# Performance work log

Hardware: AMD Instinct MI355X
Metric: run time of the kernel (lower is better)

Reference implementation:

```python
import jax, jax.numpy as jnp
import numpy as np

N = 1_000_000
C = 128
NUM_GROUPS = 100_000


def setup_inputs() -> dict:
    key = jax.random.key(0)
    k1, k2, k3 = jax.random.split(key, 3)
    ref_bxyz = jax.random.normal(k1, (N, 4), dtype=jnp.float32)
    ref_feat = jax.random.normal(k2, (N, C), dtype=jnp.float32)
    group_ids = jax.random.randint(k3, (N,), 0, NUM_GROUPS, dtype=jnp.int64)
    return {"ref_bxyz": ref_bxyz, "ref_feat": ref_feat, "group_ids": group_ids}


def reference(ref_bxyz, ref_feat, group_ids):
    # scatter-mean over groups, then gather back to each point
    num_groups = NUM_GROUPS  # static (original uses group_ids.max()+1)
    sums = jax.ops.segment_sum(ref_feat, group_ids, num_segments=num_groups)  # [G, C]
    counts = jax.ops.segment_sum(
        jnp.ones((ref_feat.shape[0],), dtype=ref_feat.dtype), group_ids,
        num_segments=num_groups)  # [G]
    group_mean = sums / jnp.maximum(counts, 1.0)[:, None]  # [G, C]
    return group_mean[group_ids]  # [N, C]
```

## Files before the change

### kernel.cpp

```cpp
#include <hip/hip_runtime.h>

#define NPTS 1000000
#define CH 128
#define NG 100000
#define SCAN_CHUNK 1024
#define NB ((NG + SCAN_CHUNK - 1) / SCAN_CHUNK)


__global__ void hist_kernel(const int* __restrict__ gid, int* __restrict__ cnt) {
    int i = blockIdx.x * blockDim.x + threadIdx.x;
    if (i < NPTS) atomicAdd(&cnt[gid[i]], 1);
}

__global__ void scan_blocks_kernel(const int* __restrict__ cnt, int* __restrict__ off,
                                   int* __restrict__ bsum) {
    __shared__ int lds[256];
    int t = threadIdx.x;
    int base = blockIdx.x * SCAN_CHUNK + t * 4;
    int a0 = 0, a1 = 0, a2 = 0, a3 = 0;
    if (base + 0 < NG) a0 = cnt[base + 0];
    if (base + 1 < NG) a1 = cnt[base + 1];
    if (base + 2 < NG) a2 = cnt[base + 2];
    if (base + 3 < NG) a3 = cnt[base + 3];
    lds[t] = a0 + a1 + a2 + a3;
    __syncthreads();
    for (int d = 1; d < 256; d <<= 1) {
        int v = (t >= d) ? lds[t - d] : 0;
        __syncthreads();
        lds[t] += v;
        __syncthreads();
    }
    int excl = (t == 0) ? 0 : lds[t - 1];
    if (t == 255) bsum[blockIdx.x] = lds[255];
    if (base + 0 < NG) off[base + 0] = excl;
    if (base + 1 < NG) off[base + 1] = excl + a0;
    if (base + 2 < NG) off[base + 2] = excl + a0 + a1;
    if (base + 3 < NG) off[base + 3] = excl + a0 + a1 + a2;
}

__global__ void scan_bsum_kernel(int* __restrict__ bsum) {
    __shared__ int lds[128];
    int t = threadIdx.x;
    int v = (t < NB) ? bsum[t] : 0;
    lds[t] = v;
    __syncthreads();
    for (int d = 1; d < 128; d <<= 1) {
        int u = (t >= d) ? lds[t - d] : 0;
        __syncthreads();
        lds[t] += u;
        __syncthreads();
    }
    int excl = (t == 0) ? 0 : lds[t - 1];
    if (t < NB) bsum[t] = excl;
}

__global__ void fill_kernel(const int* __restrict__ gid, const int* __restrict__ off,
                            const int* __restrict__ bsum, int* __restrict__ cursor,
                            int* __restrict__ idx) {
    int i = blockIdx.x * blockDim.x + threadIdx.x;
    if (i < NPTS) {
        int g = gid[i];
        int s = atomicAdd(&cursor[g], 1);
        idx[off[g] + bsum[g >> 10] + s] = i;
    }
}

__global__ void reduce_kernel(const float* __restrict__ feat, const int* __restrict__ idx,
                              const int* __restrict__ off, const int* __restrict__ bsum,
                              const int* __restrict__ cnt, float* __restrict__ means) {
    long long t = (long long)blockIdx.x * blockDim.x + threadIdx.x;
    int g = (int)(t >> 6);
    int lane = (int)(t & 63);
    if (g >= NG) return;
    int o = off[g] + bsum[g >> 10];
    int n = cnt[g];
    float2 a0 = make_float2(0.f, 0.f), a1 = make_float2(0.f, 0.f);
    int j = 0;
    for (; j + 2 <= n; j += 2) {
        int p0 = idx[o + j];
        int p1 = idx[o + j + 1];
        float2 v0 = ((const float2*)(feat + (long long)p0 * CH))[lane];
        float2 v1 = ((const float2*)(feat + (long long)p1 * CH))[lane];
        a0.x += v0.x; a0.y += v0.y;
        a1.x += v1.x; a1.y += v1.y;
    }
    if (j < n) {
        int p = idx[o + j];
        float2 v = ((const float2*)(feat + (long long)p * CH))[lane];
        a0.x += v.x; a0.y += v.y;
    }
    float inv = 1.0f / fmaxf((float)n, 1.0f);
    float2 r = make_float2((a0.x + a1.x) * inv, (a0.y + a1.y) * inv);
    ((float2*)(means + (long long)g * CH))[lane] = r;
}

__global__ void gather_mean_kernel(const float* __restrict__ means,
                                   const int* __restrict__ gid,
                                   float* __restrict__ out) {
    long long t = (long long)blockIdx.x * blockDim.x + threadIdx.x;
    int point = (int)(t >> 5);
    int sub = (int)(t & 31);
    if (point >= NPTS) return;
    int g = gid[point];
    float4 v = ((const float4*)(means + (long long)g * CH))[sub];
    ((float4*)(out + (long long)point * CH))[sub] = v;
}


__global__ void accum_kernel(const float* __restrict__ feat,
                             const int* __restrict__ gid,
                             float* __restrict__ sums,
                             float* __restrict__ counts) {
    long long t = (long long)blockIdx.x * blockDim.x + threadIdx.x;
    int point = (int)(t >> 5);
    int sub = (int)(t & 31);
    if (point >= NPTS) return;
    int g = gid[point];
    const float4 v = ((const float4*)(feat + (long long)point * CH))[sub];
    float* dst = sums + (long long)g * CH + sub * 4;
    atomicAdd(dst + 0, v.x);
    atomicAdd(dst + 1, v.y);
    atomicAdd(dst + 2, v.z);
    atomicAdd(dst + 3, v.w);
    if (sub == 0) atomicAdd(counts + g, 1.0f);
}

__global__ void inv_kernel(float* __restrict__ counts) {
    int g = blockIdx.x * blockDim.x + threadIdx.x;
    if (g < NG) counts[g] = 1.0f / fmaxf(counts[g], 1.0f);
}

__global__ void gather_kernel(const float* __restrict__ sums,
                              const float* __restrict__ inv,
                              const int* __restrict__ gid,
                              float* __restrict__ out) {
    long long t = (long long)blockIdx.x * blockDim.x + threadIdx.x;
    int point = (int)(t >> 5);
    int sub = (int)(t & 31);
    if (point >= NPTS) return;
    int g = gid[point];
    float ic = inv[g];
    float4 v = ((const float4*)(sums + (long long)g * CH))[sub];
    v.x *= ic; v.y *= ic; v.z *= ic; v.w *= ic;
    ((float4*)(out + (long long)point * CH))[sub] = v;
}


extern "C" void kernel_launch(void* const* d_in, const int* in_sizes, int n_in,
                              void* d_out, int out_size, void* d_ws, size_t ws_size,
                              hipStream_t stream) {
    const float* feat = (const float*)d_in[1];
    const int* gid = (const int*)d_in[2];
    float* out = (float*)d_out;

    char* p = (char*)d_ws;
    float* means = (float*)p;          p += (size_t)NG * CH * sizeof(float);
    int* idx     = (int*)p;            p += (size_t)NPTS * sizeof(int);
    int* cnt     = (int*)p;            p += (size_t)NG * sizeof(int);
    int* off     = (int*)p;            p += (size_t)NG * sizeof(int);
    int* cursor  = (int*)p;            p += (size_t)NG * sizeof(int);
    int* bsum    = (int*)p;            p += 128 * sizeof(int);
    size_t need = (size_t)(p - (char*)d_ws);

    const int block = 256;

    if (ws_size >= need) {
        hipMemsetAsync(cnt, 0, (size_t)NG * sizeof(int) * 3 + 128 * sizeof(int), stream);

        hist_kernel<<<(NPTS + block - 1) / block, block, 0, stream>>>(gid, cnt);
        scan_blocks_kernel<<<NB, 256, 0, stream>>>(cnt, off, bsum);
        scan_bsum_kernel<<<1, 128, 0, stream>>>(bsum);
        fill_kernel<<<(NPTS + block - 1) / block, block, 0, stream>>>(gid, off, bsum, cursor, idx);

        int rgrid = (int)(((long long)NG * 64 + block - 1) / block);
        reduce_kernel<<<rgrid, block, 0, stream>>>(feat, idx, off, bsum, cnt, means);

        int ggrid = (int)(((long long)NPTS * 32 + block - 1) / block);
        gather_mean_kernel<<<ggrid, block, 0, stream>>>(means, gid, out);
    } else {
        float* sums = (float*)d_ws;
        float* counts = sums + (long long)NG * CH;
        size_t zero_bytes = ((size_t)NG * CH + NG) * sizeof(float);
        hipMemsetAsync(d_ws, 0, zero_bytes, stream);

        long long total = (long long)NPTS * 32;
        int grid = (int)((total + block - 1) / block);
        accum_kernel<<<grid, block, 0, stream>>>(feat, gid, sums, counts);
        inv_kernel<<<(NG + block - 1) / block, block, 0, stream>>>(counts);
        gather_kernel<<<grid, block, 0, stream>>>(sums, counts, gid, out);
    }
}
```

Baseline: 1.030 ms.

## Fuse group mean reduction with scatter to output rows, drop means buffer

The reduce kernel now writes each group's mean directly to every member point's output row, eliminating the intermediate means array and the separate gather kernel. Point indices for a group are loaded once per wave and broadcast via shuffles, and group offsets are precomputed into a goff array by a new small kernel, simplifying the fill kernel. This removes one full write and random re-read of the group means plus a gid read, at the cost of scattered row writes issued from the reduce wave.

```diff
diff --git a/kernel.cpp b/kernel.cpp
--- a/kernel.cpp
+++ b/kernel.cpp
@@ -54,56 +54,72 @@
     if (t < NB) bsum[t] = excl;
 }
 
-__global__ void fill_kernel(const int* __restrict__ gid, const int* __restrict__ off,
-                            const int* __restrict__ bsum, int* __restrict__ cursor,
+__global__ void fixup_init_kernel(const int* __restrict__ off, const int* __restrict__ bsum,
+                                  int* __restrict__ goff, int* __restrict__ cursor) {
+    int i = blockIdx.x * blockDim.x + threadIdx.x;
+    if (i < NG) {
+        int v = off[i] + bsum[i >> 10];
+        goff[i] = v;
+        cursor[i] = v;
+    }
+}
+
+__global__ void fill_kernel(const int* __restrict__ gid, int* __restrict__ cursor,
                             int* __restrict__ idx) {
     int i = blockIdx.x * blockDim.x + threadIdx.x;
     if (i < NPTS) {
-        int g = gid[i];
-        int s = atomicAdd(&cursor[g], 1);
-        idx[off[g] + bsum[g >> 10] + s] = i;
-    }
-}
-
-__global__ void reduce_kernel(const float* __restrict__ feat, const int* __restrict__ idx,
-                              const int* __restrict__ off, const int* __restrict__ bsum,
-                              const int* __restrict__ cnt, float* __restrict__ means) {
+        int s = atomicAdd(&cursor[gid[i]], 1);
+        idx[s] = i;
+    }
+}
+
+__global__ void reduce_scatter_kernel(const float* __restrict__ feat,
+                                      const int* __restrict__ idx,
+                                      const int* __restrict__ goff,
+                                      const int* __restrict__ cnt,
+                                      float* __restrict__ out) {
     long long t = (long long)blockIdx.x * blockDim.x + threadIdx.x;
     int g = (int)(t >> 6);
     int lane = (int)(t & 63);
     if (g >= NG) return;
-    int o = off[g] + bsum[g >> 10];
+    int o = goff[g];
     int n = cnt[g];
+    if (n == 0) return;
+    int pv = (lane < n) ? idx[o + lane] : 0;
+    int nw = (n < 64) ? n : 64;
+
     float2 a0 = make_float2(0.f, 0.f), a1 = make_float2(0.f, 0.f);
     int j = 0;
-    for (; j + 2 <= n; j += 2) {
-        int p0 = idx[o + j];
-        int p1 = idx[o + j + 1];
+    for (; j + 2 <= nw; j += 2) {
+        int p0 = __shfl(pv, j);
+        int p1 = __shfl(pv, j + 1);
         float2 v0 = ((const float2*)(feat + (long long)p0 * CH))[lane];
         float2 v1 = ((const float2*)(feat + (long long)p1 * CH))[lane];
         a0.x += v0.x; a0.y += v0.y;
         a1.x += v1.x; a1.y += v1.y;
     }
-    if (j < n) {
-        int p = idx[o + j];
+    if (j < nw) {
+        int p = __shfl(pv, j);
         float2 v = ((const float2*)(feat + (long long)p * CH))[lane];
         a0.x += v.x; a0.y += v.y;
     }
-    float inv = 1.0f / fmaxf((float)n, 1.0f);
+    for (int k = 64; k < n; ++k) {
+        int p = idx[o + k];
+        float2 v = ((const float2*)(feat + (long long)p * CH))[lane];
+        a0.x += v.x; a0.y += v.y;
+    }
+
+    float inv = 1.0f / (float)n;
     float2 r = make_float2((a0.x + a1.x) * inv, (a0.y + a1.y) * inv);
-    ((float2*)(means + (long long)g * CH))[lane] = r;
-}
-
-__global__ void gather_mean_kernel(const float* __restrict__ means,
-                                   const int* __restrict__ gid,
-                                   float* __restrict__ out) {
-    long long t = (long long)blockIdx.x * blockDim.x + threadIdx.x;
-    int point = (int)(t >> 5);
-    int sub = (int)(t & 31);
-    if (point >= NPTS) return;
-    int g = gid[point];
-    float4 v = ((const float4*)(means + (long long)g * CH))[sub];
-    ((float4*)(out + (long long)point * CH))[sub] = v;
+
+    for (j = 0; j < nw; ++j) {
+        int p = __shfl(pv, j);
+        ((float2*)(out + (long long)p * CH))[lane] = r;
+    }
+    for (int k = 64; k < n; ++k) {
+        int p = idx[o + k];
+        ((float2*)(out + (long long)p * CH))[lane] = r;
+    }
 }
 
 
@@ -154,29 +170,27 @@
     float* out = (float*)d_out;
 
     char* p = (char*)d_ws;
-    float* means = (float*)p;          p += (size_t)NG * CH * sizeof(float);
-    int* idx     = (int*)p;            p += (size_t)NPTS * sizeof(int);
-    int* cnt     = (int*)p;            p += (size_t)NG * sizeof(int);
-    int* off     = (int*)p;            p += (size_t)NG * sizeof(int);
-    int* cursor  = (int*)p;            p += (size_t)NG * sizeof(int);
-    int* bsum    = (int*)p;            p += 128 * sizeof(int);
+    int* idx    = (int*)p;  p += (size_t)NPTS * sizeof(int);
+    int* cnt    = (int*)p;  p += (size_t)NG * sizeof(int);
+    int* off    = (int*)p;  p += (size_t)NG * sizeof(int);
+    int* goff   = (int*)p;  p += (size_t)NG * sizeof(int);
+    int* cursor = (int*)p;  p += (size_t)NG * sizeof(int);
+    int* bsum   = (int*)p;  p += 128 * sizeof(int);
     size_t need = (size_t)(p - (char*)d_ws);
 
     const int block = 256;
 
     if (ws_size >= need) {
-        hipMemsetAsync(cnt, 0, (size_t)NG * sizeof(int) * 3 + 128 * sizeof(int), stream);
+        hipMemsetAsync(cnt, 0, (size_t)NG * sizeof(int), stream);
 
         hist_kernel<<<(NPTS + block - 1) / block, block, 0, stream>>>(gid, cnt);
         scan_blocks_kernel<<<NB, 256, 0, stream>>>(cnt, off, bsum);
         scan_bsum_kernel<<<1, 128, 0, stream>>>(bsum);
-        fill_kernel<<<(NPTS + block - 1) / block, block, 0, stream>>>(gid, off, bsum, cursor, idx);
+        fixup_init_kernel<<<(NG + block - 1) / block, block, 0, stream>>>(off, bsum, goff, cursor);
+        fill_kernel<<<(NPTS + block - 1) / block, block, 0, stream>>>(gid, cursor, idx);
 
         int rgrid = (int)(((long long)NG * 64 + block - 1) / block);
-        reduce_kernel<<<rgrid, block, 0, stream>>>(feat, idx, off, bsum, cnt, means);
-
-        int ggrid = (int)(((long long)NPTS * 32 + block - 1) / block);
-        gather_mean_kernel<<<ggrid, block, 0, stream>>>(means, gid, out);
+        reduce_scatter_kernel<<<rgrid, block, 0, stream>>>(feat, idx, goff, cnt, out);
     } else {
         float* sums = (float*)d_ws;
         float* counts = sums + (long long)NG * CH;
```

Measured after the change: 964.3 us. 6.4% less time.
